# Kernel tuning notes

Measured on AMD Instinct MI355X. Metric: run time of the kernel, lower is better.

Reference implementation:

```python
import jax, jax.numpy as jnp
import numpy as np

HIDDEN = 768
NUM_HEADS = 12
HEAD_DIM = HIDDEN // NUM_HEADS  # 64


def setup_inputs() -> dict:
    key = jax.random.key(0)
    ks = jax.random.split(key, 7)
    B, S = 2, 4096
    scale = 1.0 / np.sqrt(HIDDEN)
    return {
        "hidden_states": jax.random.normal(ks[0], (B, S, HIDDEN), dtype=jnp.float32),
        "Wq": jax.random.normal(ks[1], (HIDDEN, HIDDEN), dtype=jnp.float32) * scale,
        "bq": jnp.zeros((HIDDEN,), dtype=jnp.float32),
        "Wk": jax.random.normal(ks[2], (HIDDEN, HIDDEN), dtype=jnp.float32) * scale,
        "bk": jnp.zeros((HIDDEN,), dtype=jnp.float32),
        "Wv": jax.random.normal(ks[3], (HIDDEN, HIDDEN), dtype=jnp.float32) * scale,
        "bv": jnp.zeros((HIDDEN,), dtype=jnp.float32),
    }


def _split_heads(x):
    # [B, S, H] -> [B, heads, S, head_dim]
    B, S, _ = x.shape
    return x.reshape(B, S, NUM_HEADS, HEAD_DIM).transpose(0, 2, 1, 3)


def reference(hidden_states, Wq, bq, Wk, bk, Wv, bv):
    q = _split_heads(hidden_states @ Wq + bq)  # [B, h, S, d]
    k = _split_heads(hidden_states @ Wk + bk)
    v = _split_heads(hidden_states @ Wv + bv)
    scores = jnp.einsum("bhqd,bhkd->bhqk", q, k) / np.sqrt(HEAD_DIM)
    probs = jax.nn.softmax(scores, axis=-1)  # [B, h, S, S] materialized (eager attn)
    ctx = jnp.einsum("bhqk,bhkd->bhqd", probs, v)
    B, _, S, _ = ctx.shape
    return ctx.transpose(0, 2, 1, 3).reshape(B, S, HIDDEN)
```

## Files before the change

kernel.cpp:

```cpp
#include <hip/hip_runtime.h>
#include <hip/hip_bf16.h>

typedef unsigned short ushort_t;
typedef __attribute__((ext_vector_type(4))) float f32x4;
typedef __attribute__((ext_vector_type(8))) __bf16 bfrag;
typedef __attribute__((ext_vector_type(4))) __bf16 bf4;

#define MFMA16(a,b,c) __builtin_amdgcn_mfma_f32_16x16x32_bf16((a),(b),(c),0,0,0)

#define HID 768
#define NH 12
#define SEQ 4096
#define QSCALE 0.18033688011112042f

__device__ __forceinline__ unsigned short f2bf(float x) {
  union { float f; unsigned u; } v; v.f = x;
  unsigned r = v.u + 0x7fffu + ((v.u >> 16) & 1u);
  return (unsigned short)(r >> 16);
}

typedef const unsigned char __attribute__((address_space(1)))* gas1_t;
typedef unsigned char __attribute__((address_space(3)))* las3_t;
__device__ __forceinline__ void gload_lds16(const void* g, void* l) {
  __builtin_amdgcn_global_load_lds((gas1_t)(unsigned long long)g,
                                   (las3_t)(unsigned)(unsigned long long)l,
                                   16, 0, 0);
}

__device__ __forceinline__ f32x4 zero4() { f32x4 z = {0.f, 0.f, 0.f, 0.f}; return z; }

__global__ __launch_bounds__(256) void cvt_hidden(const float* __restrict__ hs,
                                                  ushort_t* __restrict__ A) {
  int i = blockIdx.x * 256 + threadIdx.x;
  float4 v = ((const float4*)hs)[i];
  ushort4 o;
  o.x = f2bf(v.x); o.y = f2bf(v.y); o.z = f2bf(v.z); o.w = f2bf(v.w);
  ((ushort4*)A)[i] = o;
}

__global__ __launch_bounds__(256) void transpose_w(const float* __restrict__ Wq,
                                                   const float* __restrict__ Wk,
                                                   const float* __restrict__ Wv,
                                                   ushort_t* __restrict__ Wt) {
  const int z = blockIdx.z;
  const float* W = (z == 0) ? Wq : ((z == 1) ? Wk : Wv);
  const int k0 = blockIdx.x * 64, n0 = blockIdx.y * 64;
  __shared__ float tile[64][65];
  const int t = threadIdx.x;
  const int c4 = (t & 15) * 4;
  const int r = t >> 4;
#pragma unroll
  for (int it = 0; it < 4; ++it) {
    int rr = r + it * 16;
    float4 v = *(const float4*)&W[(size_t)(k0 + rr) * HID + n0 + c4];
    tile[c4 + 0][rr] = v.x; tile[c4 + 1][rr] = v.y;
    tile[c4 + 2][rr] = v.z; tile[c4 + 3][rr] = v.w;
  }
  __syncthreads();
#pragma unroll
  for (int it = 0; it < 4; ++it) {
    int nl = r + it * 16;
    ushort4 o;
    o.x = f2bf(tile[nl][c4 + 0]); o.y = f2bf(tile[nl][c4 + 1]);
    o.z = f2bf(tile[nl][c4 + 2]); o.w = f2bf(tile[nl][c4 + 3]);
    *(ushort4*)&Wt[((size_t)z * HID + n0 + nl) * HID + k0 + c4] = o;
  }
}

__global__ __launch_bounds__(256) void qkv_gemm(const ushort_t* __restrict__ A,
                                                const ushort_t* __restrict__ Wt,
                                                const float* __restrict__ bq,
                                                const float* __restrict__ bk,
                                                const float* __restrict__ bv,
                                                ushort_t* __restrict__ Qh,
                                                ushort_t* __restrict__ Kh,
                                                ushort_t* __restrict__ Vt) {
  __shared__ ushort_t Als[128 * 64];
  __shared__ ushort_t Bls[128 * 64];
  const int z = blockIdx.z;
  const int m0 = blockIdx.x * 128, n0 = blockIdx.y * 128;
  const ushort_t* Wz = Wt + (size_t)z * HID * HID;
  const float* bias = (z == 0) ? bq : ((z == 1) ? bk : bv);
  const int t = threadIdx.x, w = t >> 6, lane = t & 63;
  const int g = lane >> 4, qc = lane & 15;
  const int srow = lane >> 3, sch = lane & 7;
  const int wm = w >> 1, wn = w & 1;

  f32x4 acc[4][4];
#pragma unroll
  for (int mt = 0; mt < 4; ++mt)
#pragma unroll
    for (int nt = 0; nt < 4; ++nt) acc[mt][nt] = zero4();

  for (int kt = 0; kt < 12; ++kt) {
    const int k0 = kt * 64;
#pragma unroll
    for (int i = 0; i < 4; ++i) {
      int row = w * 32 + i * 8 + srow;
      int chA = sch ^ (srow & 7);
      gload_lds16(&A[(size_t)(m0 + row) * HID + k0 + chA * 8],
                  &Als[(w * 32 + i * 8) * 64]);
      gload_lds16(&Wz[(size_t)(n0 + row) * HID + k0 + chA * 8],
                  &Bls[(w * 32 + i * 8) * 64]);
    }
    __syncthreads();
#pragma unroll
    for (int kk = 0; kk < 2; ++kk) {
      bfrag af[4], bf_[4];
#pragma unroll
      for (int mt = 0; mt < 4; ++mt) {
        int row = wm * 64 + mt * 16 + qc;
        af[mt] = *(const bfrag*)((const char*)Als + row * 128 +
                                 (((kk * 4 + g) ^ (qc & 7)) << 4));
      }
#pragma unroll
      for (int nt = 0; nt < 4; ++nt) {
        int row = wn * 64 + nt * 16 + qc;
        bf_[nt] = *(const bfrag*)((const char*)Bls + row * 128 +
                                  (((kk * 4 + g) ^ (qc & 7)) << 4));
      }
#pragma unroll
      for (int mt = 0; mt < 4; ++mt)
#pragma unroll
        for (int nt = 0; nt < 4; ++nt)
          acc[mt][nt] = MFMA16(af[mt], bf_[nt], acc[mt][nt]);
    }
    __syncthreads();
  }

#pragma unroll
  for (int mt = 0; mt < 4; ++mt) {
#pragma unroll
    for (int nt = 0; nt < 4; ++nt) {
      int n = n0 + wn * 64 + nt * 16 + qc;
      int head = n >> 6, d = n & 63;
      float bb = bias[n];
      int mB = m0 + wm * 64 + mt * 16 + 4 * g;
      int bidx = mB >> 12, s0 = mB & 4095;
      f32x4 a = acc[mt][nt];
      if (z == 2) {
        ushort4 o;
        o.x = f2bf(a[0] + bb); o.y = f2bf(a[1] + bb);
        o.z = f2bf(a[2] + bb); o.w = f2bf(a[3] + bb);
        *(ushort4*)&Vt[((size_t)((bidx * NH + head) * 64 + d)) * SEQ + s0] = o;
      } else {
        ushort_t* dst = (z == 0) ? Qh : Kh;
        float sc = (z == 0) ? QSCALE : 1.0f;
        size_t base = (size_t)(bidx * NH + head) * SEQ;
#pragma unroll
        for (int i = 0; i < 4; ++i)
          dst[(base + s0 + i) * 64 + d] = f2bf((a[i] + bb) * sc);
      }
    }
  }
}

__global__ __launch_bounds__(256, 3) void attn_kernel(const ushort_t* __restrict__ Qh,
                                                      const ushort_t* __restrict__ Kh,
                                                      const ushort_t* __restrict__ Vt,
                                                      float* __restrict__ out) {
  const int bh = blockIdx.y;
  const int b = bh / NH, head = bh - b * NH;
  const int t = threadIdx.x, w = t >> 6, lane = t & 63;
  const int g = lane >> 4, qc = lane & 15;
  const ushort_t* Qb = Qh + (size_t)bh * SEQ * 64;
  const ushort_t* Kb = Kh + (size_t)bh * SEQ * 64;
  const ushort_t* Vb = Vt + (size_t)bh * 64 * SEQ;
  const int q0 = blockIdx.x * 128 + w * 32;

  __shared__ ushort_t Kls[2][4096];
  __shared__ ushort_t Vls[2][4096];
  __shared__ ushort_t Pls[4][2][1024];

  int jr[2], jc[2];
#pragma unroll
  for (int i = 0; i < 2; ++i) {
    int j = w * 128 + i * 64 + lane;
    jr[i] = j >> 3;
    jc[i] = (j & 7) ^ (jr[i] & 7);
  }

  bfrag qv[2][2];
#pragma unroll
  for (int qf = 0; qf < 2; ++qf)
#pragma unroll
    for (int dd = 0; dd < 2; ++dd)
      qv[qf][dd] = *(const bfrag*)&Qb[(size_t)(q0 + qf * 16 + qc) * 64 + dd * 32 + g * 8];

  f32x4 o[2][4];
  f32x4 lacc[2];
#pragma unroll
  for (int qf = 0; qf < 2; ++qf) {
    lacc[qf] = zero4();
#pragma unroll
    for (int dt = 0; dt < 4; ++dt) o[qf][dt] = zero4();
  }
  bfrag ones;
#pragma unroll
  for (int j = 0; j < 8; ++j) ones[j] = (__bf16)1.0f;

#pragma unroll
  for (int i = 0; i < 2; ++i) {
    gload_lds16(&Kb[(size_t)jr[i] * 64 + jc[i] * 8], &Kls[0][(w * 128 + i * 64) * 8]);
    gload_lds16(&Vb[(size_t)jr[i] * SEQ + jc[i] * 8], &Vls[0][(w * 128 + i * 64) * 8]);
  }

  for (int kt = 0; kt < 64; ++kt) {
    const int cur = kt & 1;
    __syncthreads();
    const int kbn = (kt == 63) ? 0 : (kt + 1) * 64;
#pragma unroll
    for (int i = 0; i < 2; ++i) {
      gload_lds16(&Kb[(size_t)(kbn + jr[i]) * 64 + jc[i] * 8],
                  &Kls[cur ^ 1][(w * 128 + i * 64) * 8]);
      gload_lds16(&Vb[(size_t)jr[i] * SEQ + kbn + jc[i] * 8],
                  &Vls[cur ^ 1][(w * 128 + i * 64) * 8]);
    }
    const ushort_t* Kc = Kls[cur];
    const ushort_t* Vc = Vls[cur];

#pragma unroll
    for (int qf = 0; qf < 2; ++qf) {
      char* Pw = (char*)&Pls[w][qf][0];
#pragma unroll
      for (int ks = 0; ks < 4; ++ks) {
        const int r = ks * 16 + qc;
        bfrag ak0 = *(const bfrag*)&Kc[r * 64 + ((g ^ (qc & 7)) * 8)];
        bfrag ak1 = *(const bfrag*)&Kc[r * 64 + (((4 + g) ^ (qc & 7)) * 8)];
        f32x4 zz = zero4();
        zz = MFMA16(ak0, qv[qf][0], zz);
        zz = MFMA16(ak1, qv[qf][1], zz);
        bf4 p4;
        p4[0] = (__bf16)__builtin_amdgcn_exp2f(zz[0]);
        p4[1] = (__bf16)__builtin_amdgcn_exp2f(zz[1]);
        p4[2] = (__bf16)__builtin_amdgcn_exp2f(zz[2]);
        p4[3] = (__bf16)__builtin_amdgcn_exp2f(zz[3]);
        *(bf4*)(Pw + qc * 128 + ((ks * 32 + g * 8) ^ ((qc & 7) << 4))) = p4;
      }
    }

#pragma unroll
    for (int kk = 0; kk < 2; ++kk) {
      bfrag av[4];
#pragma unroll
      for (int dt = 0; dt < 4; ++dt)
        av[dt] = *(const bfrag*)&Vc[(dt * 16 + qc) * 64 + (((4 * kk + g) ^ (qc & 7)) * 8)];
#pragma unroll
      for (int qf = 0; qf < 2; ++qf) {
        const char* Pw = (const char*)&Pls[w][qf][0];
        bfrag bp = *(const bfrag*)(Pw + qc * 128 + ((kk * 64 + g * 16) ^ ((qc & 7) << 4)));
#pragma unroll
        for (int dt = 0; dt < 4; ++dt)
          o[qf][dt] = MFMA16(av[dt], bp, o[qf][dt]);
        lacc[qf] = MFMA16(ones, bp, lacc[qf]);
      }
    }
  }

#pragma unroll
  for (int qf = 0; qf < 2; ++qf) {
    float inv = 1.0f / lacc[qf][0];
    int qrow = q0 + qf * 16 + qc;
    float* orow = out + (size_t)(b * SEQ + qrow) * HID + head * 64;
#pragma unroll
    for (int dt = 0; dt < 4; ++dt) {
      float4 vv;
      vv.x = o[qf][dt][0] * inv; vv.y = o[qf][dt][1] * inv;
      vv.z = o[qf][dt][2] * inv; vv.w = o[qf][dt][3] * inv;
      *(float4*)(orow + dt * 16 + 4 * g) = vv;
    }
  }
}

extern "C" void kernel_launch(void* const* d_in, const int* in_sizes, int n_in,
                              void* d_out, int out_size, void* d_ws, size_t ws_size,
                              hipStream_t stream) {
  (void)in_sizes; (void)n_in; (void)out_size; (void)ws_size;
  const float* hs = (const float*)d_in[0];
  const float* Wq = (const float*)d_in[1];
  const float* bq = (const float*)d_in[2];
  const float* Wk = (const float*)d_in[3];
  const float* bk = (const float*)d_in[4];
  const float* Wv = (const float*)d_in[5];
  const float* bv = (const float*)d_in[6];
  float* out = (float*)d_out;

  char* ws = (char*)d_ws;
  ushort_t* Abf = (ushort_t*)ws;
  ushort_t* Wt  = (ushort_t*)(ws + 12582912);
  ushort_t* Qh  = (ushort_t*)(ws + 12582912 + 3538944);
  ushort_t* Kh  = Qh + 6291456;
  ushort_t* Vt  = Kh + 6291456;

  cvt_hidden<<<6144, 256, 0, stream>>>(hs, Abf);
  transpose_w<<<dim3(12, 12, 3), 256, 0, stream>>>(Wq, Wk, Wv, Wt);
  qkv_gemm<<<dim3(64, 6, 3), 256, 0, stream>>>(Abf, Wt, bq, bk, bv, Qh, Kh, Vt);
  attn_kernel<<<dim3(32, 24), 256, 0, stream>>>(Qh, Kh, Vt, out);
}
```

Measured before the change: 179.8 us.

## Keep softmax probabilities in registers by permuting V layout to match MFMA fragments

The attention kernel no longer stages exponentiated scores through shared memory. The QKV projection now writes V with a permuted sequence ordering, so the score MFMA output fragments can be packed directly into PV operand fragments. It also adds explicit vmcnt(0) drains before barriers and skips the redundant prefetch on the last tile. This removes the LDS write/read round trip for P, at the cost of tying the V layout to the fragment mapping, with a correctness risk if the permutation is wrong.

```diff
diff --git a/kernel.cpp b/kernel.cpp
--- a/kernel.cpp
+++ b/kernel.cpp
@@ -4,7 +4,6 @@
 typedef unsigned short ushort_t;
 typedef __attribute__((ext_vector_type(4))) float f32x4;
 typedef __attribute__((ext_vector_type(8))) __bf16 bfrag;
-typedef __attribute__((ext_vector_type(4))) __bf16 bf4;
 
 #define MFMA16(a,b,c) __builtin_amdgcn_mfma_f32_16x16x32_bf16((a),(b),(c),0,0,0)
 
@@ -12,6 +11,8 @@
 #define NH 12
 #define SEQ 4096
 #define QSCALE 0.18033688011112042f
+
+#define DRAIN_VMEM() asm volatile("s_waitcnt vmcnt(0)" ::: "memory")
 
 __device__ __forceinline__ unsigned short f2bf(float x) {
   union { float f; unsigned u; } v; v.f = x;
@@ -103,6 +104,7 @@
       gload_lds16(&Wz[(size_t)(n0 + row) * HID + k0 + chA * 8],
                   &Bls[(w * 32 + i * 8) * 64]);
     }
+    DRAIN_VMEM();
     __syncthreads();
 #pragma unroll
     for (int kk = 0; kk < 2; ++kk) {
@@ -142,7 +144,8 @@
         ushort4 o;
         o.x = f2bf(a[0] + bb); o.y = f2bf(a[1] + bb);
         o.z = f2bf(a[2] + bb); o.w = f2bf(a[3] + bb);
-        *(ushort4*)&Vt[((size_t)((bidx * NH + head) * 64 + d)) * SEQ + s0] = o;
+        int scol = (s0 & ~31) | (((s0 >> 2) & 3) << 3) | (((s0 >> 4) & 1) << 2);
+        *(ushort4*)&Vt[((size_t)((bidx * NH + head) * 64 + d)) * SEQ + scol] = o;
       } else {
         ushort_t* dst = (z == 0) ? Qh : Kh;
         float sc = (z == 0) ? QSCALE : 1.0f;
@@ -170,7 +173,6 @@
 
   __shared__ ushort_t Kls[2][4096];
   __shared__ ushort_t Vls[2][4096];
-  __shared__ ushort_t Pls[4][2][1024];
 
   int jr[2], jc[2];
 #pragma unroll
@@ -207,52 +209,57 @@
 
   for (int kt = 0; kt < 64; ++kt) {
     const int cur = kt & 1;
+    DRAIN_VMEM();
     __syncthreads();
-    const int kbn = (kt == 63) ? 0 : (kt + 1) * 64;
-#pragma unroll
-    for (int i = 0; i < 2; ++i) {
-      gload_lds16(&Kb[(size_t)(kbn + jr[i]) * 64 + jc[i] * 8],
-                  &Kls[cur ^ 1][(w * 128 + i * 64) * 8]);
-      gload_lds16(&Vb[(size_t)jr[i] * SEQ + kbn + jc[i] * 8],
-                  &Vls[cur ^ 1][(w * 128 + i * 64) * 8]);
+    if (kt < 63) {
+      const int kbn = (kt + 1) * 64;
+#pragma unroll
+      for (int i = 0; i < 2; ++i) {
+        gload_lds16(&Kb[(size_t)(kbn + jr[i]) * 64 + jc[i] * 8],
+                    &Kls[cur ^ 1][(w * 128 + i * 64) * 8]);
+        gload_lds16(&Vb[(size_t)jr[i] * SEQ + kbn + jc[i] * 8],
+                    &Vls[cur ^ 1][(w * 128 + i * 64) * 8]);
+      }
     }
     const ushort_t* Kc = Kls[cur];
     const ushort_t* Vc = Vls[cur];
 
+    bfrag ak[4][2];
+#pragma unroll
+    for (int s = 0; s < 4; ++s) {
+      const int r = s * 16 + qc;
+      ak[s][0] = *(const bfrag*)&Kc[r * 64 + ((g ^ (qc & 7)) * 8)];
+      ak[s][1] = *(const bfrag*)&Kc[r * 64 + (((4 + g) ^ (qc & 7)) * 8)];
+    }
+
+    bfrag bpq[2][2];
 #pragma unroll
     for (int qf = 0; qf < 2; ++qf) {
-      char* Pw = (char*)&Pls[w][qf][0];
-#pragma unroll
-      for (int ks = 0; ks < 4; ++ks) {
-        const int r = ks * 16 + qc;
-        bfrag ak0 = *(const bfrag*)&Kc[r * 64 + ((g ^ (qc & 7)) * 8)];
-        bfrag ak1 = *(const bfrag*)&Kc[r * 64 + (((4 + g) ^ (qc & 7)) * 8)];
+      f32x4 st[4];
+#pragma unroll
+      for (int s = 0; s < 4; ++s) {
         f32x4 zz = zero4();
-        zz = MFMA16(ak0, qv[qf][0], zz);
-        zz = MFMA16(ak1, qv[qf][1], zz);
-        bf4 p4;
-        p4[0] = (__bf16)__builtin_amdgcn_exp2f(zz[0]);
-        p4[1] = (__bf16)__builtin_amdgcn_exp2f(zz[1]);
-        p4[2] = (__bf16)__builtin_amdgcn_exp2f(zz[2]);
-        p4[3] = (__bf16)__builtin_amdgcn_exp2f(zz[3]);
-        *(bf4*)(Pw + qc * 128 + ((ks * 32 + g * 8) ^ ((qc & 7) << 4))) = p4;
-      }
+        zz = MFMA16(ak[s][0], qv[qf][0], zz);
+        st[s] = MFMA16(ak[s][1], qv[qf][1], zz);
+      }
+#pragma unroll
+      for (int i = 0; i < 4; ++i) {
+        bpq[qf][0][i]     = (__bf16)__builtin_amdgcn_exp2f(st[0][i]);
+        bpq[qf][0][4 + i] = (__bf16)__builtin_amdgcn_exp2f(st[1][i]);
+        bpq[qf][1][i]     = (__bf16)__builtin_amdgcn_exp2f(st[2][i]);
+        bpq[qf][1][4 + i] = (__bf16)__builtin_amdgcn_exp2f(st[3][i]);
+      }
+      lacc[qf] = MFMA16(ones, bpq[qf][0], lacc[qf]);
+      lacc[qf] = MFMA16(ones, bpq[qf][1], lacc[qf]);
     }
 
 #pragma unroll
     for (int kk = 0; kk < 2; ++kk) {
-      bfrag av[4];
-#pragma unroll
-      for (int dt = 0; dt < 4; ++dt)
-        av[dt] = *(const bfrag*)&Vc[(dt * 16 + qc) * 64 + (((4 * kk + g) ^ (qc & 7)) * 8)];
-#pragma unroll
-      for (int qf = 0; qf < 2; ++qf) {
-        const char* Pw = (const char*)&Pls[w][qf][0];
-        bfrag bp = *(const bfrag*)(Pw + qc * 128 + ((kk * 64 + g * 16) ^ ((qc & 7) << 4)));
-#pragma unroll
-        for (int dt = 0; dt < 4; ++dt)
-          o[qf][dt] = MFMA16(av[dt], bp, o[qf][dt]);
-        lacc[qf] = MFMA16(ones, bp, lacc[qf]);
+#pragma unroll
+      for (int dt = 0; dt < 4; ++dt) {
+        bfrag av = *(const bfrag*)&Vc[(dt * 16 + qc) * 64 + (((kk * 4 + g) ^ (qc & 7)) * 8)];
+        o[0][dt] = MFMA16(av, bpq[0][kk], o[0][dt]);
+        o[1][dt] = MFMA16(av, bpq[1][kk], o[1][dt]);
       }
     }
   }
```

New measurement: 164.8 us. -8.4%, faster.
